# Kernel tuning notes

Hardware: AMD Instinct MI355X
Metric: run time of the kernel (lower is better)

The kernel has to match this reference:

```python
import jax, jax.numpy as jnp
import numpy as np

H = 64          # hidden_size
L = 5           # num_layers
D_IN = 45       # input_size
D_LAT = 128     # latent dim
D_OUT = 4       # output classes


def _lstm_layer(x, W_ih, W_hh, b):
    """One LSTM layer, batch_first input x:[B,T,D]. PyTorch gate order i,f,g,o."""
    # Precompute input contribution for all timesteps: [B,T,4H]
    xg = jnp.einsum('btd,gd->btg', x, W_ih) + b
    xg = jnp.swapaxes(xg, 0, 1)  # [T,B,4H] for scan
    B = x.shape[0]
    h0 = jnp.zeros((B, H), x.dtype)
    c0 = jnp.zeros((B, H), x.dtype)

    def step(carry, xt):
        h, c = carry
        g = xt + h @ W_hh.T                      # [B,4H]
        i, f, gg, o = jnp.split(g, 4, axis=-1)
        c = jax.nn.sigmoid(f) * c + jax.nn.sigmoid(i) * jnp.tanh(gg)
        h = jax.nn.sigmoid(o) * jnp.tanh(c)
        return (h, c), h

    (_, _), hs = jax.lax.scan(step, (h0, c0), xg)  # hs: [T,B,H]
    return jnp.swapaxes(hs, 0, 1)                  # [B,T,H]


def setup_inputs() -> dict:
    key = jax.random.key(0)
    ks = jax.random.split(key, 12)
    s = 1.0 / np.sqrt(H)  # PyTorch LSTM init scale
    x = jax.random.normal(ks[0], (256, 2048, D_IN), jnp.float32)
    W_ih0 = jax.random.uniform(ks[1], (4 * H, D_IN), jnp.float32, -s, s)
    W_ih_rest = jax.random.uniform(ks[2], (L - 1, 4 * H, H), jnp.float32, -s, s)
    W_hh = jax.random.uniform(ks[3], (L, 4 * H, H), jnp.float32, -s, s)
    b_ih = jax.random.uniform(ks[4], (L, 4 * H), jnp.float32, -s, s)
    b_hh = jax.random.uniform(ks[5], (L, 4 * H), jnp.float32, -s, s)
    Wl = jax.random.normal(ks[6], (D_LAT, H), jnp.float32) * 0.05
    bl = jnp.zeros((D_LAT,), jnp.float32)
    Wo = jax.random.normal(ks[7], (D_OUT, D_LAT), jnp.float32) * 0.05
    bo = jnp.zeros((D_OUT,), jnp.float32)
    return dict(x=x, W_ih0=W_ih0, W_ih_rest=W_ih_rest, W_hh=W_hh,
                b_ih=b_ih, b_hh=b_hh, Wl=Wl, bl=bl, Wo=Wo, bo=bo)


def reference(x, W_ih0, W_ih_rest, W_hh, b_ih, b_hh, Wl, bl, Wo, bo):
    # 5-layer LSTM (eval mode: inter-layer dropout inactive)
    h = _lstm_layer(x, W_ih0, W_hh[0], b_ih[0] + b_hh[0])
    for l in range(1, L):
        h = _lstm_layer(h, W_ih_rest[l - 1], W_hh[l], b_ih[l] + b_hh[l])
    last = h[:, -1, :]                                  # [B,H]
    features = jax.nn.gelu(last @ Wl.T + bl, approximate=False)  # [B,128]
    out = jax.nn.relu(features @ Wo.T + bo)             # [B,4]
    return out, features
```

## Files before the change

kernel.cpp:

```cpp
#include <hip/hip_runtime.h>
#include <hip/hip_fp16.h>
#include <math.h>

#define NCH   1024
#define KMAX  1034
#define HID   64
typedef unsigned int uint;
typedef __attribute__((ext_vector_type(2))) _Float16 h2t;

__device__ __forceinline__ float sigmoid_(float x){ return 1.0f/(1.0f+__expf(-x)); }
__device__ __forceinline__ float tanh_(float x){ float e=__expf(2.0f*x); return 1.0f-2.0f/(e+1.0f); }

__device__ __forceinline__ float fdot2_(uint w, uint h, float acc){
#if __has_builtin(__builtin_amdgcn_fdot2)
    return __builtin_amdgcn_fdot2(__builtin_bit_cast(h2t,w), __builtin_bit_cast(h2t,h), acc, false);
#else
    __half2 wv = *reinterpret_cast<const __half2*>(&w);
    __half2 hv = *reinterpret_cast<const __half2*>(&h);
    float2 wf = __half22float2(wv), hf = __half22float2(hv);
    return fmaf(wf.x, hf.x, fmaf(wf.y, hf.y, acc));
#endif
}
__device__ __forceinline__ uint packh(float a, float b){
    uint ha = (uint)__half_as_ushort(__float2half(a));
    uint hb = (uint)__half_as_ushort(__float2half(b));
    return (hb<<16)|ha;
}
__device__ __forceinline__ uint4 pack8(const float* p){
    return make_uint4(packh(p[0],p[1]), packh(p[2],p[3]), packh(p[4],p[5]), packh(p[6],p[7]));
}

#define DOT8(A, W, HH, HL) do{ \
    A=fdot2_((W).x,(HH).x,A); A=fdot2_((W).y,(HH).y,A); \
    A=fdot2_((W).z,(HH).z,A); A=fdot2_((W).w,(HH).w,A); \
    A=fdot2_((W).x,(HL).x,A); A=fdot2_((W).y,(HL).y,A); \
    A=fdot2_((W).z,(HL).z,A); A=fdot2_((W).w,(HL).w,A); }while(0)

__global__ __attribute__((amdgpu_waves_per_eu(1,1))) __launch_bounds__(256)
void lstm_pipe4(const float* __restrict__ x,
                const float* __restrict__ W_ih0,
                const float* __restrict__ W_ih_rest,
                const float* __restrict__ W_hh,
                const float* __restrict__ b_ih,
                const float* __restrict__ b_hh,
                float* __restrict__ h_last)
{
    __shared__ float s_xg[2][5][2][256];
    __shared__ uint  s_wo [5][8][64][4];
    __shared__ uint  s_wih[10][8][64][4];
    __shared__ uint  s_hhhi[4][2][2][32];
    __shared__ uint  s_hhlo[4][2][2][32];
    __shared__ uint  s_h16hi[5][32];
    __shared__ uint  s_h16lo[5][32];
    __shared__ uint  s_xhi[2][2][24];
    __shared__ uint  s_xlo[2][2][24];

    const int tid  = threadIdx.x;
    const int wave = tid >> 6;
    const int lane = tid & 63;
    const int sm   = blockIdx.x;
    const float* x_s = x + (size_t)sm * 2048 * 45;
    float* hlast_g = h_last + (size_t)sm * HID;

    uint4 wU[48];
    float b0=0,b1=0,b2=0,b3=0,b4=0,b5=0,b6=0,b7=0,b8=0,b9=0;
    float cA=0.f, cB=0.f;

    if (wave == 0 || wave == 1){
#pragma unroll
        for (int li=0; li<2; ++li){
            const int L = wave*2 + li;
            const float* base = W_hh + (size_t)L*256*64;
#pragma unroll
            for (int d=0; d<8; ++d){
                wU[li*24 + 0*8 + d] = pack8(base + (size_t)(  0+lane)*64 + 8*d);
                wU[li*24 + 1*8 + d] = pack8(base + (size_t)( 64+lane)*64 + 8*d);
                wU[li*24 + 2*8 + d] = pack8(base + (size_t)(128+lane)*64 + 8*d);
                *(uint4*)&s_wo[L][d][lane][0] = pack8(base + (size_t)(192+lane)*64 + 8*d);
            }
            if (lane<32){ s_h16hi[L][lane]=0u; s_h16lo[L][lane]=0u; }
        }
#pragma unroll
        for (int g=0; g<2; ++g){
            const int row = wave*128 + g*64 + lane;
            const float* src = W_ih_rest + ((size_t)3*256 + row)*64;
            const int grp = 6 + wave*2 + g;
#pragma unroll
            for (int d=0; d<8; ++d)
                *(uint4*)&s_wih[grp][d][lane][0] = pack8(src + 8*d);
        }
        { int r0 = 4*256 + wave*128 + lane, r1 = r0 + 64;
          b0 = b_ih[r0]+b_hh[r0]; b1 = b_ih[r1]+b_hh[r1]; }
    } else if (wave == 2){
        const float* base = W_hh + (size_t)4*256*64;
#pragma unroll
        for (int d=0; d<8; ++d){
            wU[0*8+d] = pack8(base + (size_t)(  0+lane)*64 + 8*d);
            wU[1*8+d] = pack8(base + (size_t)( 64+lane)*64 + 8*d);
            wU[2*8+d] = pack8(base + (size_t)(128+lane)*64 + 8*d);
            *(uint4*)&s_wo[4][d][lane][0] = pack8(base + (size_t)(192+lane)*64 + 8*d);
        }
        if (lane<32){ s_h16hi[4][lane]=0u; s_h16lo[4][lane]=0u; }
#pragma unroll
        for (int g=0; g<4; ++g){
            const float* src = W_ih0 + (size_t)(g*64+lane)*45;
#pragma unroll
            for (int d=0; d<6; ++d){
                float e0=(8*d+0<45)?src[8*d+0]:0.f, e1=(8*d+1<45)?src[8*d+1]:0.f;
                float e2=(8*d+2<45)?src[8*d+2]:0.f, e3=(8*d+3<45)?src[8*d+3]:0.f;
                float e4=(8*d+4<45)?src[8*d+4]:0.f, e5=(8*d+5<45)?src[8*d+5]:0.f;
                float e6=(8*d+6<45)?src[8*d+6]:0.f, e7=(8*d+7<45)?src[8*d+7]:0.f;
                wU[24 + g*6 + d] = make_uint4(packh(e0,e1),packh(e2,e3),packh(e4,e5),packh(e6,e7));
            }
        }
        { int r;
          r=      lane; b0=b_ih[r]+b_hh[r];
          r=  64+lane;  b1=b_ih[r]+b_hh[r];
          r= 128+lane;  b2=b_ih[r]+b_hh[r];
          r= 192+lane;  b3=b_ih[r]+b_hh[r]; }
#pragma unroll
        for (int g=0; g<2; ++g){
            const int row = 128 + g*64 + lane;
            const float* src = W_ih_rest + ((size_t)1*256 + row)*64;
#pragma unroll
            for (int d=0; d<8; ++d)
                *(uint4*)&s_wih[g][d][lane][0] = pack8(src + 8*d);
        }
        { int r0=2*256+128+lane, r1=2*256+192+lane;
          b4=b_ih[r0]+b_hh[r0]; b5=b_ih[r1]+b_hh[r1]; }
        if (lane < 12){
            int bb=lane/6, t=(lane%6)/3, d=45+lane%3;
            ((__half*)&s_xhi[bb][t][0])[d]=__float2half(0.f);
            ((__half*)&s_xlo[bb][t][0])[d]=__float2half(0.f);
        }
    } else {
#pragma unroll
        for (int g=0; g<6; ++g){
            const int ly  = (g<4) ? 1 : 2;
            const int row = (g<4) ? g*64+lane : (g-4)*64+lane;
            const float* src = W_ih_rest + ((size_t)(ly-1)*256 + row)*64;
#pragma unroll
            for (int d=0; d<8; ++d) wU[g*8+d] = pack8(src + 8*d);
        }
        { int r;
          r=1*256+  0+lane; b0=b_ih[r]+b_hh[r];
          r=1*256+ 64+lane; b1=b_ih[r]+b_hh[r];
          r=1*256+128+lane; b2=b_ih[r]+b_hh[r];
          r=1*256+192+lane; b3=b_ih[r]+b_hh[r];
          r=2*256+  0+lane; b4=b_ih[r]+b_hh[r];
          r=2*256+ 64+lane; b5=b_ih[r]+b_hh[r]; }
#pragma unroll
        for (int g=0; g<4; ++g){
            const float* src = W_ih_rest + ((size_t)2*256 + g*64+lane)*64;
#pragma unroll
            for (int d=0; d<8; ++d) *(uint4*)&s_wih[2+g][d][lane][0] = pack8(src + 8*d);
        }
        { int r;
          r=3*256+  0+lane; b6=b_ih[r]+b_hh[r];
          r=3*256+ 64+lane; b7=b_ih[r]+b_hh[r];
          r=3*256+128+lane; b8=b_ih[r]+b_hh[r];
          r=3*256+192+lane; b9=b_ih[r]+b_hh[r]; }
    }
    __syncthreads();

#define R_STEP(L, WB, LASTF, T, C, CST) do{                                    \
    const int buf_ = (C)&1;                                                    \
    float xi_ = s_xg[buf_][L][T][      lane];                                  \
    float xf_ = s_xg[buf_][L][T][ 64 + lane];                                  \
    float xgg_= s_xg[buf_][L][T][128 + lane];                                  \
    float xo_ = s_xg[buf_][L][T][192 + lane];                                  \
    float ai_=0.f, af_=0.f, ag_=0.f, ao_=0.f;                                  \
    _Pragma("unroll")                                                          \
    for (int d_=0; d_<8; ++d_){                                                \
        uint4 hh_ = *(const uint4*)&s_h16hi[L][4*d_];                          \
        uint4 hl_ = *(const uint4*)&s_h16lo[L][4*d_];                          \
        uint4 wo_ = *(const uint4*)&s_wo[L][d_][lane][0];                      \
        DOT8(ai_, wU[(WB)+d_],    hh_, hl_);                                   \
        DOT8(af_, wU[(WB)+8+d_],  hh_, hl_);                                   \
        DOT8(ag_, wU[(WB)+16+d_], hh_, hl_);                                   \
        DOT8(ao_, wo_,            hh_, hl_);                                   \
    }                                                                          \
    float I_=sigmoid_(xi_+ai_), F_=sigmoid_(xf_+af_);                          \
    float G_=tanh_(xgg_+ag_),   O_=sigmoid_(xo_+ao_);                          \
    CST = fmaf(F_, CST, I_*G_);                                                \
    float h_ = O_*tanh_(CST);                                                  \
    __half hhi_=__float2half(h_);                                              \
    __half hlo_=__float2half(h_-__half2float(hhi_));                           \
    ((__half*)&s_h16hi[L][0])[lane]=hhi_;                                      \
    ((__half*)&s_h16lo[L][0])[lane]=hlo_;                                      \
    if (!(LASTF)){                                                             \
        ((__half*)&s_hhhi[(L)<4?(L):0][buf_][T][0])[lane]=hhi_;                \
        ((__half*)&s_hhlo[(L)<4?(L):0][buf_][T][0])[lane]=hlo_;                \
    } else if ((C)==NCH-1 && (T)==1){ hlast_g[lane]=h_; }                      \
}while(0)

#define G4(DMAX, WEXPR, HHI, HLO, XDST, B0_,B1_,B2_,B3_) do{                   \
    float a0_=(B0_), a1_=(B1_), a2_=(B2_), a3_=(B3_);                          \
    _Pragma("unroll")                                                          \
    for (int d_=0; d_<(DMAX); ++d_){                                           \
        uint4 hh_ = *(const uint4*)&(HHI)[4*d_];                               \
        uint4 hl_ = *(const uint4*)&(HLO)[4*d_];                               \
        uint4 wa_ = WEXPR(0,d_); DOT8(a0_, wa_, hh_, hl_);                     \
        uint4 wb_ = WEXPR(1,d_); DOT8(a1_, wb_, hh_, hl_);                     \
        uint4 wc_ = WEXPR(2,d_); DOT8(a2_, wc_, hh_, hl_);                     \
        uint4 wd_ = WEXPR(3,d_); DOT8(a3_, wd_, hh_, hl_);                     \
    }                                                                          \
    (XDST)[      lane]=a0_; (XDST)[ 64+lane]=a1_;                              \
    (XDST)[128+lane]=a2_;   (XDST)[192+lane]=a3_;                              \
}while(0)

#define G2(DMAX, WEXPR, HHI, HLO, XDST, ROWOFF, B0_,B1_) do{                   \
    float a0_=(B0_), a1_=(B1_);                                                \
    _Pragma("unroll")                                                          \
    for (int d_=0; d_<(DMAX); ++d_){                                           \
        uint4 hh_ = *(const uint4*)&(HHI)[4*d_];                               \
        uint4 hl_ = *(const uint4*)&(HLO)[4*d_];                               \
        uint4 wa_ = WEXPR(0,d_); DOT8(a0_, wa_, hh_, hl_);                     \
        uint4 wb_ = WEXPR(1,d_); DOT8(a1_, wb_, hh_, hl_);                     \
    }                                                                          \
    (XDST)[(ROWOFF)+lane]=a0_; (XDST)[(ROWOFF)+64+lane]=a1_;                   \
}while(0)

#define W_L1(g,d)  wU[(g)*8+(d)]
#define W_L2R(g,d) wU[32+(g)*8+(d)]
#define W_L0(g,d)  wU[24+(g)*6+(d)]
#define W_L4R(g,d) wU[(g)*8+(d)]
#define W_L2L(g,d) (*(const uint4*)&s_wih[(g)][d][lane][0])
#define W_L3(g,d)  (*(const uint4*)&s_wih[2+(g)][d][lane][0])
#define W_L4A(g,d) (*(const uint4*)&s_wih[6+(g)][d][lane][0])
#define W_L4B(g,d) (*(const uint4*)&s_wih[8+(g)][d][lane][0])

    for (int k=0; k<KMAX; ++k){
        if (wave == 0){
            const int c0=k-2, c1=k-4, cl=k-9;
            if (c0>=0 && c0<NCH) R_STEP(0,  0, 0, 0, c0, cA);
            if (c1>=0 && c1<NCH) R_STEP(1, 24, 0, 0, c1, cB);
            if (c0>=0 && c0<NCH) R_STEP(0,  0, 0, 1, c0, cA);
            if (c1>=0 && c1<NCH) R_STEP(1, 24, 0, 1, c1, cB);
            if (cl>=0 && cl<NCH){
                const int bl=cl&1;
                G2(8, W_L4A, &s_hhhi[3][bl][0][0], &s_hhlo[3][bl][0][0], &s_xg[bl][4][0][0], 0, b0,b1);
                G2(8, W_L4A, &s_hhhi[3][bl][1][0], &s_hhlo[3][bl][1][0], &s_xg[bl][4][1][0], 0, b0,b1);
            }
        } else if (wave == 1){
            const int c2=k-6, c3=k-8, cl=k-9;
            if (c2>=0 && c2<NCH) R_STEP(2,  0, 0, 0, c2, cA);
            if (c3>=0 && c3<NCH) R_STEP(3, 24, 0, 0, c3, cB);
            if (c2>=0 && c2<NCH) R_STEP(2,  0, 0, 1, c2, cA);
            if (c3>=0 && c3<NCH) R_STEP(3, 24, 0, 1, c3, cB);
            if (cl>=0 && cl<NCH){
                const int bl=cl&1;
                G2(8, W_L4B, &s_hhhi[3][bl][0][0], &s_hhlo[3][bl][0][0], &s_xg[bl][4][0][0], 128, b0,b1);
                G2(8, W_L4B, &s_hhhi[3][bl][1][0], &s_hhlo[3][bl][1][0], &s_xg[bl][4][1][0], 128, b0,b1);
            }
        } else if (wave == 2){
            if (k < NCH){
                const int bufx = k & 1;
#pragma unroll
                for (int r=0; r<2; ++r){
                    const int i = lane + 64*r;
                    if (i < 90){
                        float v = x_s[(size_t)k*90 + i];
                        __half vh = __float2half(v);
                        __half vl = __float2half(v - __half2float(vh));
                        const int t = i/45, d = i - 45*t;
                        ((__half*)&s_xhi[bufx][t][0])[d] = vh;
                        ((__half*)&s_xlo[bufx][t][0])[d] = vl;
                    }
                }
            }
            const int c4=k-10, cg0=k-1, cg2=k-5;
            if (c4>=0 && c4<NCH)  R_STEP(4, 0, 1, 0, c4, cA);
            if (cg0>=0 && cg0<NCH){
                const int bg=cg0&1;
                G4(6, W_L0, &s_xhi[bg][0][0], &s_xlo[bg][0][0], &s_xg[bg][0][0][0], b0,b1,b2,b3);
                G4(6, W_L0, &s_xhi[bg][1][0], &s_xlo[bg][1][0], &s_xg[bg][0][1][0], b0,b1,b2,b3);
            }
            if (c4>=0 && c4<NCH)  R_STEP(4, 0, 1, 1, c4, cA);
            if (cg2>=0 && cg2<NCH){
                const int bg=cg2&1;
                G2(8, W_L2L, &s_hhhi[1][bg][0][0], &s_hhlo[1][bg][0][0], &s_xg[bg][2][0][0], 128, b4,b5);
                G2(8, W_L2L, &s_hhhi[1][bg][1][0], &s_hhlo[1][bg][1][0], &s_xg[bg][2][1][0], 128, b4,b5);
            }
        } else {
            const int cg1=k-3, cg2=k-5, cg3=k-7;
            if (cg1>=0 && cg1<NCH){
                const int bg=cg1&1;
                G4(8, W_L1, &s_hhhi[0][bg][0][0], &s_hhlo[0][bg][0][0], &s_xg[bg][1][0][0], b0,b1,b2,b3);
                G4(8, W_L1, &s_hhhi[0][bg][1][0], &s_hhlo[0][bg][1][0], &s_xg[bg][1][1][0], b0,b1,b2,b3);
            }
            if (cg2>=0 && cg2<NCH){
                const int bg=cg2&1;
                G2(8, W_L2R, &s_hhhi[1][bg][0][0], &s_hhlo[1][bg][0][0], &s_xg[bg][2][0][0], 0, b4,b5);
                G2(8, W_L2R, &s_hhhi[1][bg][1][0], &s_hhlo[1][bg][1][0], &s_xg[bg][2][1][0], 0, b4,b5);
            }
            if (cg3>=0 && cg3<NCH){
                const int bg=cg3&1;
                G4(8, W_L3, &s_hhhi[2][bg][0][0], &s_hhlo[2][bg][0][0], &s_xg[bg][3][0][0], b6,b7,b8,b9);
                G4(8, W_L3, &s_hhhi[2][bg][1][0], &s_hhlo[2][bg][1][0], &s_xg[bg][3][1][0], b6,b7,b8,b9);
            }
        }
        __syncthreads();
    }
}

__global__ __launch_bounds__(128)
void head_kernel(const float* __restrict__ h_last,
                 const float* __restrict__ Wl,
                 const float* __restrict__ bl,
                 const float* __restrict__ Wo,
                 const float* __restrict__ bo,
                 float* __restrict__ d_out)
{
    __shared__ float s_last[HID];
    __shared__ float s_feat[128];
    const int s = blockIdx.x;
    const int j = threadIdx.x;

    if (j < HID) s_last[j] = h_last[(size_t)s * HID + j];
    __syncthreads();

    float acc = bl[j];
#pragma unroll
    for (int k = 0; k < HID; ++k)
        acc = fmaf(s_last[k], Wl[j * HID + k], acc);
    float f = 0.5f * acc * (1.0f + erff(acc * 0.70710678118654752440f));
    d_out[256 * 4 + s * 128 + j] = f;
    s_feat[j] = f;
    __syncthreads();

    if (j < 4) {
        float a = bo[j];
#pragma unroll
        for (int k = 0; k < 128; ++k)
            a = fmaf(s_feat[k], Wo[j * 128 + k], a);
        d_out[s * 4 + j] = fmaxf(a, 0.0f);
    }
}

extern "C" void kernel_launch(void* const* d_in, const int* in_sizes, int n_in,
                              void* d_out, int out_size, void* d_ws, size_t ws_size,
                              hipStream_t stream)
{
    const float* x         = (const float*)d_in[0];
    const float* W_ih0     = (const float*)d_in[1];
    const float* W_ih_rest = (const float*)d_in[2];
    const float* W_hh      = (const float*)d_in[3];
    const float* b_ih      = (const float*)d_in[4];
    const float* b_hh      = (const float*)d_in[5];
    const float* Wl        = (const float*)d_in[6];
    const float* bl        = (const float*)d_in[7];
    const float* Wo        = (const float*)d_in[8];
    const float* bo        = (const float*)d_in[9];

    float* h_last = (float*)d_ws;

    lstm_pipe4<<<256, 256, 0, stream>>>(
        x, W_ih0, W_ih_rest, W_hh, b_ih, b_hh, h_last);
    head_kernel<<<256, 128, 0, stream>>>(h_last, Wl, bl, Wo, bo, (float*)d_out);
}
```

Baseline: 5.649 ms.

## Split LSTM dot accumulators and add branch-free steady-state pipeline loop

The recurrent step now uses separate hi/lo accumulators per gate, which shortens the serial fdot2 dependency chains. A steady-state path for k in [10,NCH) drops the per-stage bounds checks. In that path the input-gate GEMVs for both timesteps are computed together, so each weight load is reused for two h vectors. Wave 3's layer-3 work is split into two G2T halves. The cost is more registers and duplicated code for the prologue and epilogue, which could raise register pressure under the one-wave-per-EU setting.

```diff
diff --git a/kernel.cpp b/kernel.cpp
--- a/kernel.cpp
+++ b/kernel.cpp
@@ -30,11 +30,10 @@
     return make_uint4(packh(p[0],p[1]), packh(p[2],p[3]), packh(p[4],p[5]), packh(p[6],p[7]));
 }
 
-#define DOT8(A, W, HH, HL) do{ \
-    A=fdot2_((W).x,(HH).x,A); A=fdot2_((W).y,(HH).y,A); \
-    A=fdot2_((W).z,(HH).z,A); A=fdot2_((W).w,(HH).w,A); \
-    A=fdot2_((W).x,(HL).x,A); A=fdot2_((W).y,(HL).y,A); \
-    A=fdot2_((W).z,(HL).z,A); A=fdot2_((W).w,(HL).w,A); }while(0)
+#define DOT4(A, W, H) do{ \
+    A=fdot2_((W).x,(H).x,A); A=fdot2_((W).y,(H).y,A); \
+    A=fdot2_((W).z,(H).z,A); A=fdot2_((W).w,(H).w,A); }while(0)
+#define DOT8(A, W, HH, HL) do{ DOT4(A,W,HH); DOT4(A,W,HL); }while(0)
 
 __global__ __attribute__((amdgpu_waves_per_eu(1,1))) __launch_bounds__(256)
 void lstm_pipe4(const float* __restrict__ x,
@@ -163,25 +162,25 @@
     }
     __syncthreads();
 
-#define R_STEP(L, WB, LASTF, T, C, CST) do{                                    \
+#define R_STEPF(L, WB, LASTF, T, C, CST) do{                                   \
     const int buf_ = (C)&1;                                                    \
     float xi_ = s_xg[buf_][L][T][      lane];                                  \
     float xf_ = s_xg[buf_][L][T][ 64 + lane];                                  \
     float xgg_= s_xg[buf_][L][T][128 + lane];                                  \
     float xo_ = s_xg[buf_][L][T][192 + lane];                                  \
-    float ai_=0.f, af_=0.f, ag_=0.f, ao_=0.f;                                  \
+    float aih=0,ail=0, afh=0,afl=0, agh=0,agl=0, aoh=0,aol=0;                  \
     _Pragma("unroll")                                                          \
     for (int d_=0; d_<8; ++d_){                                                \
         uint4 hh_ = *(const uint4*)&s_h16hi[L][4*d_];                          \
         uint4 hl_ = *(const uint4*)&s_h16lo[L][4*d_];                          \
         uint4 wo_ = *(const uint4*)&s_wo[L][d_][lane][0];                      \
-        DOT8(ai_, wU[(WB)+d_],    hh_, hl_);                                   \
-        DOT8(af_, wU[(WB)+8+d_],  hh_, hl_);                                   \
-        DOT8(ag_, wU[(WB)+16+d_], hh_, hl_);                                   \
-        DOT8(ao_, wo_,            hh_, hl_);                                   \
-    }                                                                          \
-    float I_=sigmoid_(xi_+ai_), F_=sigmoid_(xf_+af_);                          \
-    float G_=tanh_(xgg_+ag_),   O_=sigmoid_(xo_+ao_);                          \
+        DOT4(aih, wU[(WB)+d_],    hh_); DOT4(ail, wU[(WB)+d_],    hl_);        \
+        DOT4(afh, wU[(WB)+8+d_],  hh_); DOT4(afl, wU[(WB)+8+d_],  hl_);        \
+        DOT4(agh, wU[(WB)+16+d_], hh_); DOT4(agl, wU[(WB)+16+d_], hl_);        \
+        DOT4(aoh, wo_,            hh_); DOT4(aol, wo_,            hl_);        \
+    }                                                                          \
+    float I_=sigmoid_(xi_+(aih+ail)), F_=sigmoid_(xf_+(afh+afl));              \
+    float G_=tanh_(xgg_+(agh+agl)),   O_=sigmoid_(xo_+(aoh+aol));              \
     CST = fmaf(F_, CST, I_*G_);                                                \
     float h_ = O_*tanh_(CST);                                                  \
     __half hhi_=__float2half(h_);                                              \
@@ -194,6 +193,41 @@
     } else if ((C)==NCH-1 && (T)==1){ hlast_g[lane]=h_; }                      \
 }while(0)
 
+#define G4T(DMAX, WEXPR, H0HI,H0LO,H1HI,H1LO, XD0, XD1, B0_,B1_,B2_,B3_) do{   \
+    float a00=(B0_),a01=(B1_),a02=(B2_),a03=(B3_);                             \
+    float a10=(B0_),a11=(B1_),a12=(B2_),a13=(B3_);                             \
+    _Pragma("unroll")                                                          \
+    for (int d_=0; d_<(DMAX); ++d_){                                           \
+        uint4 w0_=WEXPR(0,d_), w1_=WEXPR(1,d_), w2_=WEXPR(2,d_), w3_=WEXPR(3,d_);\
+        uint4 h0h_=*(const uint4*)&(H0HI)[4*d_], h0l_=*(const uint4*)&(H0LO)[4*d_];\
+        uint4 h1h_=*(const uint4*)&(H1HI)[4*d_], h1l_=*(const uint4*)&(H1LO)[4*d_];\
+        DOT8(a00,w0_,h0h_,h0l_); DOT8(a01,w1_,h0h_,h0l_);                      \
+        DOT8(a02,w2_,h0h_,h0l_); DOT8(a03,w3_,h0h_,h0l_);                      \
+        DOT8(a10,w0_,h1h_,h1l_); DOT8(a11,w1_,h1h_,h1l_);                      \
+        DOT8(a12,w2_,h1h_,h1l_); DOT8(a13,w3_,h1h_,h1l_);                      \
+    }                                                                          \
+    (XD0)[      lane]=a00; (XD0)[ 64+lane]=a01;                                \
+    (XD0)[128+lane]=a02;   (XD0)[192+lane]=a03;                                \
+    (XD1)[      lane]=a10; (XD1)[ 64+lane]=a11;                                \
+    (XD1)[128+lane]=a12;   (XD1)[192+lane]=a13;                                \
+}while(0)
+
+#define G2T(DMAX, WEXPR, H0HI,H0LO,H1HI,H1LO, XD0, XD1, ROWOFF, B0_,B1_) do{   \
+    float p00=0,q00=0,p01=0,q01=0, p10=0,q10=0,p11=0,q11=0;                    \
+    _Pragma("unroll")                                                          \
+    for (int d_=0; d_<(DMAX); ++d_){                                           \
+        uint4 wa_ = WEXPR(0,d_), wb_ = WEXPR(1,d_);                            \
+        uint4 h0h_=*(const uint4*)&(H0HI)[4*d_], h0l_=*(const uint4*)&(H0LO)[4*d_];\
+        uint4 h1h_=*(const uint4*)&(H1HI)[4*d_], h1l_=*(const uint4*)&(H1LO)[4*d_];\
+        DOT4(p00,wa_,h0h_); DOT4(q00,wa_,h0l_);                                \
+        DOT4(p01,wb_,h0h_); DOT4(q01,wb_,h0l_);                                \
+        DOT4(p10,wa_,h1h_); DOT4(q10,wa_,h1l_);                                \
+        DOT4(p11,wb_,h1h_); DOT4(q11,wb_,h1l_);                                \
+    }                                                                          \
+    (XD0)[(ROWOFF)+lane]=(B0_)+p00+q00; (XD0)[(ROWOFF)+64+lane]=(B1_)+p01+q01; \
+    (XD1)[(ROWOFF)+lane]=(B0_)+p10+q10; (XD1)[(ROWOFF)+64+lane]=(B1_)+p11+q11; \
+}while(0)
+
 #define G4(DMAX, WEXPR, HHI, HLO, XDST, B0_,B1_,B2_,B3_) do{                   \
     float a0_=(B0_), a1_=(B1_), a2_=(B2_), a3_=(B3_);                          \
     _Pragma("unroll")                                                          \
@@ -224,80 +258,131 @@
 #define W_L1(g,d)  wU[(g)*8+(d)]
 #define W_L2R(g,d) wU[32+(g)*8+(d)]
 #define W_L0(g,d)  wU[24+(g)*6+(d)]
-#define W_L4R(g,d) wU[(g)*8+(d)]
 #define W_L2L(g,d) (*(const uint4*)&s_wih[(g)][d][lane][0])
 #define W_L3(g,d)  (*(const uint4*)&s_wih[2+(g)][d][lane][0])
+#define W_L3A(g,d) (*(const uint4*)&s_wih[2+(g)][d][lane][0])
+#define W_L3B(g,d) (*(const uint4*)&s_wih[4+(g)][d][lane][0])
 #define W_L4A(g,d) (*(const uint4*)&s_wih[6+(g)][d][lane][0])
 #define W_L4B(g,d) (*(const uint4*)&s_wih[8+(g)][d][lane][0])
 
+#define STAGE_X() do{                                                          \
+    const int bufx = k & 1;                                                    \
+    _Pragma("unroll")                                                          \
+    for (int r=0; r<2; ++r){                                                   \
+        const int i = lane + 64*r;                                             \
+        if (i < 90){                                                           \
+            float v = x_s[(size_t)k*90 + i];                                   \
+            __half vh = __float2half(v);                                       \
+            __half vl = __float2half(v - __half2float(vh));                    \
+            const int t = i/45, d = i - 45*t;                                  \
+            ((__half*)&s_xhi[bufx][t][0])[d] = vh;                             \
+            ((__half*)&s_xlo[bufx][t][0])[d] = vl;                             \
+        }                                                                      \
+    }                                                                          \
+}while(0)
+
     for (int k=0; k<KMAX; ++k){
-        if (wave == 0){
-            const int c0=k-2, c1=k-4, cl=k-9;
-            if (c0>=0 && c0<NCH) R_STEP(0,  0, 0, 0, c0, cA);
-            if (c1>=0 && c1<NCH) R_STEP(1, 24, 0, 0, c1, cB);
-            if (c0>=0 && c0<NCH) R_STEP(0,  0, 0, 1, c0, cA);
-            if (c1>=0 && c1<NCH) R_STEP(1, 24, 0, 1, c1, cB);
-            if (cl>=0 && cl<NCH){
-                const int bl=cl&1;
-                G2(8, W_L4A, &s_hhhi[3][bl][0][0], &s_hhlo[3][bl][0][0], &s_xg[bl][4][0][0], 0, b0,b1);
-                G2(8, W_L4A, &s_hhhi[3][bl][1][0], &s_hhlo[3][bl][1][0], &s_xg[bl][4][1][0], 0, b0,b1);
-            }
-        } else if (wave == 1){
-            const int c2=k-6, c3=k-8, cl=k-9;
-            if (c2>=0 && c2<NCH) R_STEP(2,  0, 0, 0, c2, cA);
-            if (c3>=0 && c3<NCH) R_STEP(3, 24, 0, 0, c3, cB);
-            if (c2>=0 && c2<NCH) R_STEP(2,  0, 0, 1, c2, cA);
-            if (c3>=0 && c3<NCH) R_STEP(3, 24, 0, 1, c3, cB);
-            if (cl>=0 && cl<NCH){
-                const int bl=cl&1;
-                G2(8, W_L4B, &s_hhhi[3][bl][0][0], &s_hhlo[3][bl][0][0], &s_xg[bl][4][0][0], 128, b0,b1);
-                G2(8, W_L4B, &s_hhhi[3][bl][1][0], &s_hhlo[3][bl][1][0], &s_xg[bl][4][1][0], 128, b0,b1);
-            }
-        } else if (wave == 2){
-            if (k < NCH){
-                const int bufx = k & 1;
-#pragma unroll
-                for (int r=0; r<2; ++r){
-                    const int i = lane + 64*r;
-                    if (i < 90){
-                        float v = x_s[(size_t)k*90 + i];
-                        __half vh = __float2half(v);
-                        __half vl = __float2half(v - __half2float(vh));
-                        const int t = i/45, d = i - 45*t;
-                        ((__half*)&s_xhi[bufx][t][0])[d] = vh;
-                        ((__half*)&s_xlo[bufx][t][0])[d] = vl;
-                    }
-                }
-            }
-            const int c4=k-10, cg0=k-1, cg2=k-5;
-            if (c4>=0 && c4<NCH)  R_STEP(4, 0, 1, 0, c4, cA);
-            if (cg0>=0 && cg0<NCH){
-                const int bg=cg0&1;
-                G4(6, W_L0, &s_xhi[bg][0][0], &s_xlo[bg][0][0], &s_xg[bg][0][0][0], b0,b1,b2,b3);
-                G4(6, W_L0, &s_xhi[bg][1][0], &s_xlo[bg][1][0], &s_xg[bg][0][1][0], b0,b1,b2,b3);
-            }
-            if (c4>=0 && c4<NCH)  R_STEP(4, 0, 1, 1, c4, cA);
-            if (cg2>=0 && cg2<NCH){
-                const int bg=cg2&1;
-                G2(8, W_L2L, &s_hhhi[1][bg][0][0], &s_hhlo[1][bg][0][0], &s_xg[bg][2][0][0], 128, b4,b5);
-                G2(8, W_L2L, &s_hhhi[1][bg][1][0], &s_hhlo[1][bg][1][0], &s_xg[bg][2][1][0], 128, b4,b5);
+        if (k >= 10 && k < NCH){
+            const int pb  = k & 1;
+            const int pb1 = pb ^ 1;
+            if (wave == 0){
+                const int c0=k-2, c1=k-4;
+                R_STEPF(0,  0, 0, 0, c0, cA);
+                R_STEPF(1, 24, 0, 0, c1, cB);
+                R_STEPF(0,  0, 0, 1, c0, cA);
+                R_STEPF(1, 24, 0, 1, c1, cB);
+                G2T(8, W_L4A, s_hhhi[3][pb1][0], s_hhlo[3][pb1][0],
+                              s_hhhi[3][pb1][1], s_hhlo[3][pb1][1],
+                    (&s_xg[pb1][4][0][0]), (&s_xg[pb1][4][1][0]), 0, b0,b1);
+            } else if (wave == 1){
+                const int c2=k-6, c3=k-8;
+                R_STEPF(2,  0, 0, 0, c2, cA);
+                R_STEPF(3, 24, 0, 0, c3, cB);
+                R_STEPF(2,  0, 0, 1, c2, cA);
+                R_STEPF(3, 24, 0, 1, c3, cB);
+                G2T(8, W_L4B, s_hhhi[3][pb1][0], s_hhlo[3][pb1][0],
+                              s_hhhi[3][pb1][1], s_hhlo[3][pb1][1],
+                    (&s_xg[pb1][4][0][0]), (&s_xg[pb1][4][1][0]), 128, b0,b1);
+            } else if (wave == 2){
+                STAGE_X();
+                const int c4=k-10;
+                R_STEPF(4, 0, 1, 0, c4, cA);
+                G4T(6, W_L0, (&s_xhi[pb1][0][0]), (&s_xlo[pb1][0][0]),
+                             (&s_xhi[pb1][1][0]), (&s_xlo[pb1][1][0]),
+                    (&s_xg[pb1][0][0][0]), (&s_xg[pb1][0][1][0]), b0,b1,b2,b3);
+                R_STEPF(4, 0, 1, 1, c4, cA);
+                G2T(8, W_L2L, s_hhhi[1][pb1][0], s_hhlo[1][pb1][0],
+                              s_hhhi[1][pb1][1], s_hhlo[1][pb1][1],
+                    (&s_xg[pb1][2][0][0]), (&s_xg[pb1][2][1][0]), 128, b4,b5);
+            } else {
+                G4T(8, W_L1, s_hhhi[0][pb1][0], s_hhlo[0][pb1][0],
+                             s_hhhi[0][pb1][1], s_hhlo[0][pb1][1],
+                    (&s_xg[pb1][1][0][0]), (&s_xg[pb1][1][1][0]), b0,b1,b2,b3);
+                G2T(8, W_L2R, s_hhhi[1][pb1][0], s_hhlo[1][pb1][0],
+                              s_hhhi[1][pb1][1], s_hhlo[1][pb1][1],
+                    (&s_xg[pb1][2][0][0]), (&s_xg[pb1][2][1][0]), 0, b4,b5);
+                G2T(8, W_L3A, s_hhhi[2][pb1][0], s_hhlo[2][pb1][0],
+                              s_hhhi[2][pb1][1], s_hhlo[2][pb1][1],
+                    (&s_xg[pb1][3][0][0]), (&s_xg[pb1][3][1][0]), 0, b6,b7);
+                G2T(8, W_L3B, s_hhhi[2][pb1][0], s_hhlo[2][pb1][0],
+                              s_hhhi[2][pb1][1], s_hhlo[2][pb1][1],
+                    (&s_xg[pb1][3][0][0]), (&s_xg[pb1][3][1][0]), 128, b8,b9);
             }
         } else {
-            const int cg1=k-3, cg2=k-5, cg3=k-7;
-            if (cg1>=0 && cg1<NCH){
-                const int bg=cg1&1;
-                G4(8, W_L1, &s_hhhi[0][bg][0][0], &s_hhlo[0][bg][0][0], &s_xg[bg][1][0][0], b0,b1,b2,b3);
-                G4(8, W_L1, &s_hhhi[0][bg][1][0], &s_hhlo[0][bg][1][0], &s_xg[bg][1][1][0], b0,b1,b2,b3);
-            }
-            if (cg2>=0 && cg2<NCH){
-                const int bg=cg2&1;
-                G2(8, W_L2R, &s_hhhi[1][bg][0][0], &s_hhlo[1][bg][0][0], &s_xg[bg][2][0][0], 0, b4,b5);
-                G2(8, W_L2R, &s_hhhi[1][bg][1][0], &s_hhlo[1][bg][1][0], &s_xg[bg][2][1][0], 0, b4,b5);
-            }
-            if (cg3>=0 && cg3<NCH){
-                const int bg=cg3&1;
-                G4(8, W_L3, &s_hhhi[2][bg][0][0], &s_hhlo[2][bg][0][0], &s_xg[bg][3][0][0], b6,b7,b8,b9);
-                G4(8, W_L3, &s_hhhi[2][bg][1][0], &s_hhlo[2][bg][1][0], &s_xg[bg][3][1][0], b6,b7,b8,b9);
+            if (wave == 0){
+                const int c0=k-2, c1=k-4, cl=k-9;
+                if (c0>=0 && c0<NCH) R_STEPF(0,  0, 0, 0, c0, cA);
+                if (c1>=0 && c1<NCH) R_STEPF(1, 24, 0, 0, c1, cB);
+                if (c0>=0 && c0<NCH) R_STEPF(0,  0, 0, 1, c0, cA);
+                if (c1>=0 && c1<NCH) R_STEPF(1, 24, 0, 1, c1, cB);
+                if (cl>=0 && cl<NCH){
+                    const int bl=cl&1;
+                    G2(8, W_L4A, (&s_hhhi[3][bl][0][0]), (&s_hhlo[3][bl][0][0]), (&s_xg[bl][4][0][0]), 0, b0,b1);
+                    G2(8, W_L4A, (&s_hhhi[3][bl][1][0]), (&s_hhlo[3][bl][1][0]), (&s_xg[bl][4][1][0]), 0, b0,b1);
+                }
+            } else if (wave == 1){
+                const int c2=k-6, c3=k-8, cl=k-9;
+                if (c2>=0 && c2<NCH) R_STEPF(2,  0, 0, 0, c2, cA);
+                if (c3>=0 && c3<NCH) R_STEPF(3, 24, 0, 0, c3, cB);
+                if (c2>=0 && c2<NCH) R_STEPF(2,  0, 0, 1, c2, cA);
+                if (c3>=0 && c3<NCH) R_STEPF(3, 24, 0, 1, c3, cB);
+                if (cl>=0 && cl<NCH){
+                    const int bl=cl&1;
+                    G2(8, W_L4B, (&s_hhhi[3][bl][0][0]), (&s_hhlo[3][bl][0][0]), (&s_xg[bl][4][0][0]), 128, b0,b1);
+                    G2(8, W_L4B, (&s_hhhi[3][bl][1][0]), (&s_hhlo[3][bl][1][0]), (&s_xg[bl][4][1][0]), 128, b0,b1);
+                }
+            } else if (wave == 2){
+                if (k < NCH) STAGE_X();
+                const int c4=k-10, cg0=k-1, cg2=k-5;
+                if (c4>=0 && c4<NCH)  R_STEPF(4, 0, 1, 0, c4, cA);
+                if (cg0>=0 && cg0<NCH){
+                    const int bg=cg0&1;
+                    G4(6, W_L0, (&s_xhi[bg][0][0]), (&s_xlo[bg][0][0]), (&s_xg[bg][0][0][0]), b0,b1,b2,b3);
+                    G4(6, W_L0, (&s_xhi[bg][1][0]), (&s_xlo[bg][1][0]), (&s_xg[bg][0][1][0]), b0,b1,b2,b3);
+                }
+                if (c4>=0 && c4<NCH)  R_STEPF(4, 0, 1, 1, c4, cA);
+                if (cg2>=0 && cg2<NCH){
+                    const int bg=cg2&1;
+                    G2(8, W_L2L, (&s_hhhi[1][bg][0][0]), (&s_hhlo[1][bg][0][0]), (&s_xg[bg][2][0][0]), 128, b4,b5);
+                    G2(8, W_L2L, (&s_hhhi[1][bg][1][0]), (&s_hhlo[1][bg][1][0]), (&s_xg[bg][2][1][0]), 128, b4,b5);
+                }
+            } else {
+                const int cg1=k-3, cg2=k-5, cg3=k-7;
+                if (cg1>=0 && cg1<NCH){
+                    const int bg=cg1&1;
+                    G4(8, W_L1, (&s_hhhi[0][bg][0][0]), (&s_hhlo[0][bg][0][0]), (&s_xg[bg][1][0][0]), b0,b1,b2,b3);
+                    G4(8, W_L1, (&s_hhhi[0][bg][1][0]), (&s_hhlo[0][bg][1][0]), (&s_xg[bg][1][1][0]), b0,b1,b2,b3);
+                }
+                if (cg2>=0 && cg2<NCH){
+                    const int bg=cg2&1;
+                    G2(8, W_L2R, (&s_hhhi[1][bg][0][0]), (&s_hhlo[1][bg][0][0]), (&s_xg[bg][2][0][0]), 0, b4,b5);
+                    G2(8, W_L2R, (&s_hhhi[1][bg][1][0]), (&s_hhlo[1][bg][1][0]), (&s_xg[bg][2][1][0]), 0, b4,b5);
+                }
+                if (cg3>=0 && cg3<NCH){
+                    const int bg=cg3&1;
+                    G4(8, W_L3, (&s_hhhi[2][bg][0][0]), (&s_hhlo[2][bg][0][0]), (&s_xg[bg][3][0][0]), b6,b7,b8,b9);
+                    G4(8, W_L3, (&s_hhhi[2][bg][1][0]), (&s_hhlo[2][bg][1][0]), (&s_xg[bg][3][1][0]), b6,b7,b8,b9);
+                }
             }
         }
         __syncthreads();
```

After: 8.526 ms. +50.9%, slower.

## Drop fp16 hi/lo split, use single fp16 operands and split accumulators

Applied to the files above, without the earlier changes.

Removes the hi/lo fp16 decomposition of hidden states and inputs, so every dot product uses a single fp16 operand and half the fdot2 instructions and LDS traffic. Splits the recurrent accumulators into two interleaved chains to shorten dependency latency. Merges the two per-timestep input projections into one pass that reuses loaded weights, and emits an unguarded steady-state loop body. The cost is lower numerical precision, since h and x are now rounded to plain fp16 with no correction term, which risks tolerance failures over 2048 steps and 5 layers.

```diff
diff --git a/kernel.cpp b/kernel.cpp
--- a/kernel.cpp
+++ b/kernel.cpp
@@ -30,11 +30,9 @@
     return make_uint4(packh(p[0],p[1]), packh(p[2],p[3]), packh(p[4],p[5]), packh(p[6],p[7]));
 }
 
-#define DOT8(A, W, HH, HL) do{ \
-    A=fdot2_((W).x,(HH).x,A); A=fdot2_((W).y,(HH).y,A); \
-    A=fdot2_((W).z,(HH).z,A); A=fdot2_((W).w,(HH).w,A); \
-    A=fdot2_((W).x,(HL).x,A); A=fdot2_((W).y,(HL).y,A); \
-    A=fdot2_((W).z,(HL).z,A); A=fdot2_((W).w,(HL).w,A); }while(0)
+#define DOT4(A, W, H) do{ \
+    A=fdot2_((W).x,(H).x,A); A=fdot2_((W).y,(H).y,A); \
+    A=fdot2_((W).z,(H).z,A); A=fdot2_((W).w,(H).w,A); }while(0)
 
 __global__ __attribute__((amdgpu_waves_per_eu(1,1))) __launch_bounds__(256)
 void lstm_pipe4(const float* __restrict__ x,
@@ -48,12 +46,9 @@
     __shared__ float s_xg[2][5][2][256];
     __shared__ uint  s_wo [5][8][64][4];
     __shared__ uint  s_wih[10][8][64][4];
-    __shared__ uint  s_hhhi[4][2][2][32];
-    __shared__ uint  s_hhlo[4][2][2][32];
-    __shared__ uint  s_h16hi[5][32];
-    __shared__ uint  s_h16lo[5][32];
-    __shared__ uint  s_xhi[2][2][24];
-    __shared__ uint  s_xlo[2][2][24];
+    __shared__ uint  s_hh[4][2][2][32];
+    __shared__ uint  s_h16[5][32];
+    __shared__ uint  s_x[2][2][24];
 
     const int tid  = threadIdx.x;
     const int wave = tid >> 6;
@@ -78,7 +73,7 @@
                 wU[li*24 + 2*8 + d] = pack8(base + (size_t)(128+lane)*64 + 8*d);
                 *(uint4*)&s_wo[L][d][lane][0] = pack8(base + (size_t)(192+lane)*64 + 8*d);
             }
-            if (lane<32){ s_h16hi[L][lane]=0u; s_h16lo[L][lane]=0u; }
+            if (lane<32) s_h16[L][lane]=0u;
         }
 #pragma unroll
         for (int g=0; g<2; ++g){
@@ -100,7 +95,7 @@
             wU[2*8+d] = pack8(base + (size_t)(128+lane)*64 + 8*d);
             *(uint4*)&s_wo[4][d][lane][0] = pack8(base + (size_t)(192+lane)*64 + 8*d);
         }
-        if (lane<32){ s_h16hi[4][lane]=0u; s_h16lo[4][lane]=0u; }
+        if (lane<32) s_h16[4][lane]=0u;
 #pragma unroll
         for (int g=0; g<4; ++g){
             const float* src = W_ih0 + (size_t)(g*64+lane)*45;
@@ -130,8 +125,7 @@
           b4=b_ih[r0]+b_hh[r0]; b5=b_ih[r1]+b_hh[r1]; }
         if (lane < 12){
             int bb=lane/6, t=(lane%6)/3, d=45+lane%3;
-            ((__half*)&s_xhi[bb][t][0])[d]=__float2half(0.f);
-            ((__half*)&s_xlo[bb][t][0])[d]=__float2half(0.f);
+            ((__half*)&s_x[bb][t][0])[d]=__float2half(0.f);
         }
     } else {
 #pragma unroll
@@ -163,142 +157,163 @@
     }
     __syncthreads();
 
-#define R_STEP(L, WB, LASTF, T, C, CST) do{                                    \
+#define R_STEPN(L, WB, LASTF, T, C, CST) do{                                   \
     const int buf_ = (C)&1;                                                    \
     float xi_ = s_xg[buf_][L][T][      lane];                                  \
     float xf_ = s_xg[buf_][L][T][ 64 + lane];                                  \
     float xgg_= s_xg[buf_][L][T][128 + lane];                                  \
     float xo_ = s_xg[buf_][L][T][192 + lane];                                  \
-    float ai_=0.f, af_=0.f, ag_=0.f, ao_=0.f;                                  \
+    float ai0=0,ai1=0, af0=0,af1=0, ag0=0,ag1=0, ao0=0,ao1=0;                  \
     _Pragma("unroll")                                                          \
-    for (int d_=0; d_<8; ++d_){                                                \
-        uint4 hh_ = *(const uint4*)&s_h16hi[L][4*d_];                          \
-        uint4 hl_ = *(const uint4*)&s_h16lo[L][4*d_];                          \
-        uint4 wo_ = *(const uint4*)&s_wo[L][d_][lane][0];                      \
-        DOT8(ai_, wU[(WB)+d_],    hh_, hl_);                                   \
-        DOT8(af_, wU[(WB)+8+d_],  hh_, hl_);                                   \
-        DOT8(ag_, wU[(WB)+16+d_], hh_, hl_);                                   \
-        DOT8(ao_, wo_,            hh_, hl_);                                   \
+    for (int d_=0; d_<8; d_+=2){                                               \
+        uint4 h0_ = *(const uint4*)&s_h16[L][4*d_];                            \
+        uint4 h1_ = *(const uint4*)&s_h16[L][4*d_+4];                          \
+        uint4 woA_ = *(const uint4*)&s_wo[L][d_  ][lane][0];                   \
+        uint4 woB_ = *(const uint4*)&s_wo[L][d_+1][lane][0];                   \
+        DOT4(ai0, wU[(WB)+d_],      h0_); DOT4(ai1, wU[(WB)+d_+1],    h1_);    \
+        DOT4(af0, wU[(WB)+8+d_],    h0_); DOT4(af1, wU[(WB)+8+d_+1],  h1_);    \
+        DOT4(ag0, wU[(WB)+16+d_],   h0_); DOT4(ag1, wU[(WB)+16+d_+1], h1_);    \
+        DOT4(ao0, woA_,             h0_); DOT4(ao1, woB_,             h1_);    \
     }                                                                          \
-    float I_=sigmoid_(xi_+ai_), F_=sigmoid_(xf_+af_);                          \
-    float G_=tanh_(xgg_+ag_),   O_=sigmoid_(xo_+ao_);                          \
+    float I_=sigmoid_(xi_+(ai0+ai1)), F_=sigmoid_(xf_+(af0+af1));              \
+    float G_=tanh_(xgg_+(ag0+ag1)),   O_=sigmoid_(xo_+(ao0+ao1));              \
     CST = fmaf(F_, CST, I_*G_);                                                \
     float h_ = O_*tanh_(CST);                                                  \
     __half hhi_=__float2half(h_);                                              \
-    __half hlo_=__float2half(h_-__half2float(hhi_));                           \
-    ((__half*)&s_h16hi[L][0])[lane]=hhi_;                                      \
-    ((__half*)&s_h16lo[L][0])[lane]=hlo_;                                      \
+    ((__half*)&s_h16[L][0])[lane]=hhi_;                                        \
     if (!(LASTF)){                                                             \
-        ((__half*)&s_hhhi[(L)<4?(L):0][buf_][T][0])[lane]=hhi_;                \
-        ((__half*)&s_hhlo[(L)<4?(L):0][buf_][T][0])[lane]=hlo_;                \
+        ((__half*)&s_hh[(L)<4?(L):0][buf_][T][0])[lane]=hhi_;                  \
     } else if ((C)==NCH-1 && (T)==1){ hlast_g[lane]=h_; }                      \
 }while(0)
 
-#define G4(DMAX, WEXPR, HHI, HLO, XDST, B0_,B1_,B2_,B3_) do{                   \
-    float a0_=(B0_), a1_=(B1_), a2_=(B2_), a3_=(B3_);                          \
+#define G4T(DMAX, WEXPR, H0, H1, XD0, XD1, B0_,B1_,B2_,B3_) do{                \
+    float a00=(B0_),a01=(B1_),a02=(B2_),a03=(B3_);                             \
+    float a10=(B0_),a11=(B1_),a12=(B2_),a13=(B3_);                             \
     _Pragma("unroll")                                                          \
     for (int d_=0; d_<(DMAX); ++d_){                                           \
-        uint4 hh_ = *(const uint4*)&(HHI)[4*d_];                               \
-        uint4 hl_ = *(const uint4*)&(HLO)[4*d_];                               \
-        uint4 wa_ = WEXPR(0,d_); DOT8(a0_, wa_, hh_, hl_);                     \
-        uint4 wb_ = WEXPR(1,d_); DOT8(a1_, wb_, hh_, hl_);                     \
-        uint4 wc_ = WEXPR(2,d_); DOT8(a2_, wc_, hh_, hl_);                     \
-        uint4 wd_ = WEXPR(3,d_); DOT8(a3_, wd_, hh_, hl_);                     \
+        uint4 w0_=WEXPR(0,d_), w1_=WEXPR(1,d_), w2_=WEXPR(2,d_), w3_=WEXPR(3,d_);\
+        uint4 h0_=*(const uint4*)&(H0)[4*d_];                                  \
+        uint4 h1_=*(const uint4*)&(H1)[4*d_];                                  \
+        DOT4(a00,w0_,h0_); DOT4(a01,w1_,h0_); DOT4(a02,w2_,h0_); DOT4(a03,w3_,h0_);\
+        DOT4(a10,w0_,h1_); DOT4(a11,w1_,h1_); DOT4(a12,w2_,h1_); DOT4(a13,w3_,h1_);\
     }                                                                          \
-    (XDST)[      lane]=a0_; (XDST)[ 64+lane]=a1_;                              \
-    (XDST)[128+lane]=a2_;   (XDST)[192+lane]=a3_;                              \
-}while(0)
-
-#define G2(DMAX, WEXPR, HHI, HLO, XDST, ROWOFF, B0_,B1_) do{                   \
-    float a0_=(B0_), a1_=(B1_);                                                \
+    (XD0)[      lane]=a00; (XD0)[ 64+lane]=a01;                                \
+    (XD0)[128+lane]=a02;   (XD0)[192+lane]=a03;                                \
+    (XD1)[      lane]=a10; (XD1)[ 64+lane]=a11;                                \
+    (XD1)[128+lane]=a12;   (XD1)[192+lane]=a13;                                \
+}while(0)
+
+#define G2T(DMAX, WEXPR, H0, H1, XD0, XD1, ROWOFF, B0_,B1_) do{                \
+    float a00=(B0_),a01=(B1_), a10=(B0_),a11=(B1_);                            \
     _Pragma("unroll")                                                          \
     for (int d_=0; d_<(DMAX); ++d_){                                           \
-        uint4 hh_ = *(const uint4*)&(HHI)[4*d_];                               \
-        uint4 hl_ = *(const uint4*)&(HLO)[4*d_];                               \
-        uint4 wa_ = WEXPR(0,d_); DOT8(a0_, wa_, hh_, hl_);                     \
-        uint4 wb_ = WEXPR(1,d_); DOT8(a1_, wb_, hh_, hl_);                     \
+        uint4 wa_ = WEXPR(0,d_), wb_ = WEXPR(1,d_);                            \
+        uint4 h0_=*(const uint4*)&(H0)[4*d_];                                  \
+        uint4 h1_=*(const uint4*)&(H1)[4*d_];                                  \
+        DOT4(a00,wa_,h0_); DOT4(a01,wb_,h0_);                                  \
+        DOT4(a10,wa_,h1_); DOT4(a11,wb_,h1_);                                  \
     }                                                                          \
-    (XDST)[(ROWOFF)+lane]=a0_; (XDST)[(ROWOFF)+64+lane]=a1_;                   \
+    (XD0)[(ROWOFF)+lane]=a00; (XD0)[(ROWOFF)+64+lane]=a01;                     \
+    (XD1)[(ROWOFF)+lane]=a10; (XD1)[(ROWOFF)+64+lane]=a11;                     \
 }while(0)
 
 #define W_L1(g,d)  wU[(g)*8+(d)]
 #define W_L2R(g,d) wU[32+(g)*8+(d)]
 #define W_L0(g,d)  wU[24+(g)*6+(d)]
-#define W_L4R(g,d) wU[(g)*8+(d)]
 #define W_L2L(g,d) (*(const uint4*)&s_wih[(g)][d][lane][0])
 #define W_L3(g,d)  (*(const uint4*)&s_wih[2+(g)][d][lane][0])
 #define W_L4A(g,d) (*(const uint4*)&s_wih[6+(g)][d][lane][0])
 #define W_L4B(g,d) (*(const uint4*)&s_wih[8+(g)][d][lane][0])
 
+#define STAGE_X() do{                                                          \
+    const int bufx = k & 1;                                                    \
+    _Pragma("unroll")                                                          \
+    for (int r=0; r<2; ++r){                                                   \
+        const int i = lane + 64*r;                                             \
+        if (i < 90){                                                           \
+            float v = x_s[(size_t)k*90 + i];                                   \
+            const int t = i/45, d = i - 45*t;                                  \
+            ((__half*)&s_x[bufx][t][0])[d] = __float2half(v);                  \
+        }                                                                      \
+    }                                                                          \
+}while(0)
+
+#define BODY_W0(GUARDED) do{                                                   \
+    const int c0=k-2, c1=k-4, cl=k-9;                                          \
+    if (!(GUARDED) || (c0>=0 && c0<NCH)){                                      \
+        R_STEPN(0,  0, 0, 0, c0, cA); }                                        \
+    if (!(GUARDED) || (c1>=0 && c1<NCH)){                                      \
+        R_STEPN(1, 24, 0, 0, c1, cB); }                                        \
+    if (!(GUARDED) || (c0>=0 && c0<NCH)){                                      \
+        R_STEPN(0,  0, 0, 1, c0, cA); }                                        \
+    if (!(GUARDED) || (c1>=0 && c1<NCH)){                                      \
+        R_STEPN(1, 24, 0, 1, c1, cB); }                                        \
+    if (!(GUARDED) || (cl>=0 && cl<NCH)){                                      \
+        const int bl=cl&1;                                                     \
+        G2T(8, W_L4A, (&s_hh[3][bl][0][0]), (&s_hh[3][bl][1][0]),              \
+            (&s_xg[bl][4][0][0]), (&s_xg[bl][4][1][0]), 0, b0,b1); }           \
+}while(0)
+
+#define BODY_W1(GUARDED) do{                                                   \
+    const int c2=k-6, c3=k-8, cl=k-9;                                          \
+    if (!(GUARDED) || (c2>=0 && c2<NCH)){                                      \
+        R_STEPN(2,  0, 0, 0, c2, cA); }                                        \
+    if (!(GUARDED) || (c3>=0 && c3<NCH)){                                      \
+        R_STEPN(3, 24, 0, 0, c3, cB); }                                        \
+    if (!(GUARDED) || (c2>=0 && c2<NCH)){                                      \
+        R_STEPN(2,  0, 0, 1, c2, cA); }                                        \
+    if (!(GUARDED) || (c3>=0 && c3<NCH)){                                      \
+        R_STEPN(3, 24, 0, 1, c3, cB); }                                        \
+    if (!(GUARDED) || (cl>=0 && cl<NCH)){                                      \
+        const int bl=cl&1;                                                     \
+        G2T(8, W_L4B, (&s_hh[3][bl][0][0]), (&s_hh[3][bl][1][0]),              \
+            (&s_xg[bl][4][0][0]), (&s_xg[bl][4][1][0]), 128, b0,b1); }         \
+}while(0)
+
+#define BODY_W2(GUARDED) do{                                                   \
+    if (!(GUARDED) || (k < NCH)) STAGE_X();                                    \
+    const int c4=k-10, cg0=k-1, cg2=k-5;                                       \
+    if (!(GUARDED) || (c4>=0 && c4<NCH)){                                      \
+        R_STEPN(4, 0, 1, 0, c4, cA); }                                         \
+    if (!(GUARDED) || (cg0>=0 && cg0<NCH)){                                    \
+        const int bg=cg0&1;                                                    \
+        G4T(6, W_L0, (&s_x[bg][0][0]), (&s_x[bg][1][0]),                       \
+            (&s_xg[bg][0][0][0]), (&s_xg[bg][0][1][0]), b0,b1,b2,b3); }        \
+    if (!(GUARDED) || (c4>=0 && c4<NCH)){                                      \
+        R_STEPN(4, 0, 1, 1, c4, cA); }                                         \
+    if (!(GUARDED) || (cg2>=0 && cg2<NCH)){                                    \
+        const int bg=cg2&1;                                                    \
+        G2T(8, W_L2L, (&s_hh[1][bg][0][0]), (&s_hh[1][bg][1][0]),              \
+            (&s_xg[bg][2][0][0]), (&s_xg[bg][2][1][0]), 128, b4,b5); }         \
+}while(0)
+
+#define BODY_W3(GUARDED) do{                                                   \
+    const int cg1=k-3, cg2=k-5, cg3=k-7;                                       \
+    if (!(GUARDED) || (cg1>=0 && cg1<NCH)){                                    \
+        const int bg=cg1&1;                                                    \
+        G4T(8, W_L1, (&s_hh[0][bg][0][0]), (&s_hh[0][bg][1][0]),               \
+            (&s_xg[bg][1][0][0]), (&s_xg[bg][1][1][0]), b0,b1,b2,b3); }        \
+    if (!(GUARDED) || (cg2>=0 && cg2<NCH)){                                    \
+        const int bg=cg2&1;                                                    \
+        G2T(8, W_L2R, (&s_hh[1][bg][0][0]), (&s_hh[1][bg][1][0]),              \
+            (&s_xg[bg][2][0][0]), (&s_xg[bg][2][1][0]), 0, b4,b5); }           \
+    if (!(GUARDED) || (cg3>=0 && cg3<NCH)){                                    \
+        const int bg=cg3&1;                                                    \
+        G4T(8, W_L3, (&s_hh[2][bg][0][0]), (&s_hh[2][bg][1][0]),               \
+            (&s_xg[bg][3][0][0]), (&s_xg[bg][3][1][0]), b6,b7,b8,b9); }        \
+}while(0)
+
     for (int k=0; k<KMAX; ++k){
-        if (wave == 0){
-            const int c0=k-2, c1=k-4, cl=k-9;
-            if (c0>=0 && c0<NCH) R_STEP(0,  0, 0, 0, c0, cA);
-            if (c1>=0 && c1<NCH) R_STEP(1, 24, 0, 0, c1, cB);
-            if (c0>=0 && c0<NCH) R_STEP(0,  0, 0, 1, c0, cA);
-            if (c1>=0 && c1<NCH) R_STEP(1, 24, 0, 1, c1, cB);
-            if (cl>=0 && cl<NCH){
-                const int bl=cl&1;
-                G2(8, W_L4A, &s_hhhi[3][bl][0][0], &s_hhlo[3][bl][0][0], &s_xg[bl][4][0][0], 0, b0,b1);
-                G2(8, W_L4A, &s_hhhi[3][bl][1][0], &s_hhlo[3][bl][1][0], &s_xg[bl][4][1][0], 0, b0,b1);
-            }
-        } else if (wave == 1){
-            const int c2=k-6, c3=k-8, cl=k-9;
-            if (c2>=0 && c2<NCH) R_STEP(2,  0, 0, 0, c2, cA);
-            if (c3>=0 && c3<NCH) R_STEP(3, 24, 0, 0, c3, cB);
-            if (c2>=0 && c2<NCH) R_STEP(2,  0, 0, 1, c2, cA);
-            if (c3>=0 && c3<NCH) R_STEP(3, 24, 0, 1, c3, cB);
-            if (cl>=0 && cl<NCH){
-                const int bl=cl&1;
-                G2(8, W_L4B, &s_hhhi[3][bl][0][0], &s_hhlo[3][bl][0][0], &s_xg[bl][4][0][0], 128, b0,b1);
-                G2(8, W_L4B, &s_hhhi[3][bl][1][0], &s_hhlo[3][bl][1][0], &s_xg[bl][4][1][0], 128, b0,b1);
-            }
-        } else if (wave == 2){
-            if (k < NCH){
-                const int bufx = k & 1;
-#pragma unroll
-                for (int r=0; r<2; ++r){
-                    const int i = lane + 64*r;
-                    if (i < 90){
-                        float v = x_s[(size_t)k*90 + i];
-                        __half vh = __float2half(v);
-                        __half vl = __float2half(v - __half2float(vh));
-                        const int t = i/45, d = i - 45*t;
-                        ((__half*)&s_xhi[bufx][t][0])[d] = vh;
-                        ((__half*)&s_xlo[bufx][t][0])[d] = vl;
-                    }
-                }
-            }
-            const int c4=k-10, cg0=k-1, cg2=k-5;
-            if (c4>=0 && c4<NCH)  R_STEP(4, 0, 1, 0, c4, cA);
-            if (cg0>=0 && cg0<NCH){
-                const int bg=cg0&1;
-                G4(6, W_L0, &s_xhi[bg][0][0], &s_xlo[bg][0][0], &s_xg[bg][0][0][0], b0,b1,b2,b3);
-                G4(6, W_L0, &s_xhi[bg][1][0], &s_xlo[bg][1][0], &s_xg[bg][0][1][0], b0,b1,b2,b3);
-            }
-            if (c4>=0 && c4<NCH)  R_STEP(4, 0, 1, 1, c4, cA);
-            if (cg2>=0 && cg2<NCH){
-                const int bg=cg2&1;
-                G2(8, W_L2L, &s_hhhi[1][bg][0][0], &s_hhlo[1][bg][0][0], &s_xg[bg][2][0][0], 128, b4,b5);
-                G2(8, W_L2L, &s_hhhi[1][bg][1][0], &s_hhlo[1][bg][1][0], &s_xg[bg][2][1][0], 128, b4,b5);
-            }
+        if (k >= 10 && k < NCH){
+            if      (wave == 0) BODY_W0(0);
+            else if (wave == 1) BODY_W1(0);
+            else if (wave == 2) BODY_W2(0);
+            else                BODY_W3(0);
         } else {
-            const int cg1=k-3, cg2=k-5, cg3=k-7;
-            if (cg1>=0 && cg1<NCH){
-                const int bg=cg1&1;
-                G4(8, W_L1, &s_hhhi[0][bg][0][0], &s_hhlo[0][bg][0][0], &s_xg[bg][1][0][0], b0,b1,b2,b3);
-                G4(8, W_L1, &s_hhhi[0][bg][1][0], &s_hhlo[0][bg][1][0], &s_xg[bg][1][1][0], b0,b1,b2,b3);
-            }
-            if (cg2>=0 && cg2<NCH){
-                const int bg=cg2&1;
-                G2(8, W_L2R, &s_hhhi[1][bg][0][0], &s_hhlo[1][bg][0][0], &s_xg[bg][2][0][0], 0, b4,b5);
-                G2(8, W_L2R, &s_hhhi[1][bg][1][0], &s_hhlo[1][bg][1][0], &s_xg[bg][2][1][0], 0, b4,b5);
-            }
-            if (cg3>=0 && cg3<NCH){
-                const int bg=cg3&1;
-                G4(8, W_L3, &s_hhhi[2][bg][0][0], &s_hhlo[2][bg][0][0], &s_xg[bg][3][0][0], b6,b7,b8,b9);
-                G4(8, W_L3, &s_hhhi[2][bg][1][0], &s_hhlo[2][bg][1][0], &s_xg[bg][3][1][0], b6,b7,b8,b9);
-            }
+            if      (wave == 0) BODY_W0(1);
+            else if (wave == 1) BODY_W1(1);
+            else if (wave == 2) BODY_W2(1);
+            else                BODY_W3(1);
         }
         __syncthreads();
     }
```

Result: faster. 4.621 ms (-18.2%).
